# Kernel optimization log

Hardware: AMD Instinct MI355X
Metric: run time of the kernel (lower is better)

The kernel has to match this reference:

```python
import jax, jax.numpy as jnp
import numpy as np

NEG_SLOPE = 0.2

def gat_conv(x, src, dst, n_nodes, W, a_src, a_dst, bias, heads, out_c):
    # x: [N, in]; W: [in, heads*out_c]; a_src/a_dst: [heads, out_c]; bias: [heads*out_c]
    h = (x @ W).reshape(n_nodes, heads, out_c)            # [N,H,C]
    e_s = jnp.sum(h * a_src, axis=-1)                     # [N,H] per-node src score
    e_d = jnp.sum(h * a_dst, axis=-1)                     # [N,H] per-node dst score
    e = jax.nn.leaky_relu(e_s[src] + e_d[dst], NEG_SLOPE) # [E,H]
    # segment softmax over destination neighborhoods
    emax = jax.ops.segment_max(e, dst, num_segments=n_nodes)  # [N,H]
    emax = jnp.where(jnp.isfinite(emax), emax, 0.0)
    p = jnp.exp(e - emax[dst])                            # [E,H]
    denom = jax.ops.segment_sum(p, dst, num_segments=n_nodes)  # [N,H]
    alpha = p / (denom[dst] + 1e-16)                      # [E,H]
    msg = h[src] * alpha[:, :, None]                      # [E,H,C]
    out = jax.ops.segment_sum(msg, dst, num_segments=n_nodes)  # [N,H,C]
    return out.reshape(n_nodes, heads * out_c) + bias


def setup_inputs() -> dict:
    key = jax.random.key(0)
    ks = jax.random.split(key, 10)
    N, E, IN, OUT, H = 50000, 1600000, 128, 32, 2
    x = jax.random.normal(ks[0], (N, IN), dtype=jnp.float32)
    edge_index = jax.random.randint(ks[1], (2, E), 0, N, dtype=jnp.int64)
    s = 0.1
    W1 = jax.random.normal(ks[2], (IN, H * OUT), dtype=jnp.float32) * s
    a_src1 = jax.random.normal(ks[3], (H, OUT), dtype=jnp.float32) * s
    a_dst1 = jax.random.normal(ks[4], (H, OUT), dtype=jnp.float32) * s
    b1 = jnp.zeros((H * OUT,), dtype=jnp.float32)
    W2 = jax.random.normal(ks[5], (H * OUT, OUT), dtype=jnp.float32) * s
    a_src2 = jax.random.normal(ks[6], (1, OUT), dtype=jnp.float32) * s
    a_dst2 = jax.random.normal(ks[7], (1, OUT), dtype=jnp.float32) * s
    b2 = jnp.zeros((OUT,), dtype=jnp.float32)
    return {"x": x, "edge_index": edge_index, "W1": W1, "a_src1": a_src1,
            "a_dst1": a_dst1, "b1": b1, "W2": W2, "a_src2": a_src2,
            "a_dst2": a_dst2, "b2": b2}


def reference(x, edge_index, W1, a_src1, a_dst1, b1, W2, a_src2, a_dst2, b2):
    N = x.shape[0]
    # add_self_loops=True (PyG GATConv default)
    loops = jnp.arange(N, dtype=edge_index.dtype)
    ei = jnp.concatenate([edge_index, jnp.stack([loops, loops])], axis=1)
    src, dst = ei[0], ei[1]
    h = gat_conv(x, src, dst, N, W1, a_src1, a_dst1, b1, heads=2, out_c=32)
    h = jax.nn.relu(h)
    out = gat_conv(h, src, dst, N, W2, a_src2, a_dst2, b2, heads=1, out_c=32)
    return out
```

## Files before the change

kernel.cpp:

```cpp
#include <hip/hip_runtime.h>
#include <hip/hip_fp16.h>

#define NEG_SLOPE 0.2f
#define DB 128
#define NB_MAX 512
#define EPB 4096
#define CAP 8192

__global__ __launch_bounds__(256) void k_g1p(
    const float* __restrict__ x, const float* __restrict__ W,
    const float* __restrict__ a_src, const float* __restrict__ a_dst,
    __half* __restrict__ h1, float* __restrict__ es, float* __restrict__ ed, int N,
    const int* __restrict__ srcv, const int* __restrict__ dstv,
    int* __restrict__ gcur, int* __restrict__ ebuf, int E, int G1) {
  __shared__ __align__(16) char smem[32768];
  const int t = threadIdx.x;

  if ((int)blockIdx.x < G1) {
    __half* sXT = (__half*)smem;
    __half* sW  = (__half*)(smem + 16384);
    const int r0 = blockIdx.x * 64;
    {
      const float4* Wp = (const float4*)W;
#pragma unroll
      for (int i = 0; i < 8; ++i) {
        float4 v = Wp[t + i * 256];
        int fi = (t + i * 256) * 4;
        union { __half2 h2[2]; float2 f; } u;
        u.h2[0] = __float22half2_rn(make_float2(v.x, v.y));
        u.h2[1] = __float22half2_rn(make_float2(v.z, v.w));
        *(float2*)(sW + fi) = u.f;
      }
    }
    {
      int r = t & 63;
      int kq = t >> 6;
      int gr = r0 + r;
      bool ok = gr < N;
      const float* xr = x + (size_t)gr * 128;
#pragma unroll
      for (int p = 0; p < 8; ++p) {
        int k = (kq + p * 4) * 4;
        float4 v = ok ? *(const float4*)(xr + k) : make_float4(0.f, 0.f, 0.f, 0.f);
        sXT[(k + 0) * 64 + r] = __float2half(v.x);
        sXT[(k + 1) * 64 + r] = __float2half(v.y);
        sXT[(k + 2) * 64 + r] = __float2half(v.z);
        sXT[(k + 3) * 64 + r] = __float2half(v.w);
      }
    }
    __syncthreads();

    const int tx = t & 15, ty = t >> 4;
    float4 acc0 = make_float4(0.f, 0.f, 0.f, 0.f);
    float4 acc1 = acc0, acc2 = acc0, acc3 = acc0;
#pragma unroll 4
    for (int k = 0; k < 128; ++k) {
      const __half2* ap = (const __half2*)(sXT + k * 64 + ty * 4);
      const __half2* bp = (const __half2*)(sW + k * 64 + tx * 4);
      float2 a01 = __half22float2(ap[0]);
      float2 a23 = __half22float2(ap[1]);
      float2 b01 = __half22float2(bp[0]);
      float2 b23 = __half22float2(bp[1]);
      acc0.x += a01.x * b01.x; acc0.y += a01.x * b01.y; acc0.z += a01.x * b23.x; acc0.w += a01.x * b23.y;
      acc1.x += a01.y * b01.x; acc1.y += a01.y * b01.y; acc1.z += a01.y * b23.x; acc1.w += a01.y * b23.y;
      acc2.x += a23.x * b01.x; acc2.y += a23.x * b01.y; acc2.z += a23.x * b23.x; acc2.w += a23.x * b23.y;
      acc3.x += a23.y * b01.x; acc3.y += a23.y * b01.y; acc3.z += a23.y * b23.x; acc3.w += a23.y * b23.y;
    }

    float4 accs[4] = {acc0, acc1, acc2, acc3};
#pragma unroll
    for (int i = 0; i < 4; ++i) {
      int gr = r0 + ty * 4 + i;
      if (gr < N) {
        union { __half2 h[2]; float2 f; } u;
        u.h[0] = __float22half2_rn(make_float2(accs[i].x, accs[i].y));
        u.h[1] = __float22half2_rn(make_float2(accs[i].z, accs[i].w));
        *(float2*)(h1 + (size_t)gr * 64 + tx * 4) = u.f;
      }
    }

    float4 asv = *(const float4*)(a_src + tx * 4);
    float4 adv = *(const float4*)(a_dst + tx * 4);
    float esp[4], edp[4];
#pragma unroll
    for (int i = 0; i < 4; ++i) {
      esp[i] = accs[i].x * asv.x + accs[i].y * asv.y + accs[i].z * asv.z + accs[i].w * asv.w;
      edp[i] = accs[i].x * adv.x + accs[i].y * adv.y + accs[i].z * adv.z + accs[i].w * adv.w;
    }
#pragma unroll
    for (int off = 1; off <= 4; off <<= 1) {
#pragma unroll
      for (int i = 0; i < 4; ++i) {
        esp[i] += __shfl_xor(esp[i], off);
        edp[i] += __shfl_xor(edp[i], off);
      }
    }
    if ((tx & 7) == 0) {
      int hh = tx >> 3;
#pragma unroll
      for (int i = 0; i < 4; ++i) {
        int gr = r0 + ty * 4 + i;
        if (gr < N) {
          es[gr * 2 + hh] = esp[i];
          ed[gr * 2 + hh] = edp[i];
        }
      }
    }
  } else {
    int* sh    = (int*)smem;
    int* lbase = (int*)(smem + 2048);
    sh[t] = 0; sh[t + 256] = 0;
    __syncthreads();
    int base = (blockIdx.x - G1) * EPB;
    int dd[16];
#pragma unroll
    for (int i = 0; i < 16; ++i) {
      int e = base + i * 256 + t;
      dd[i] = (e < E) ? dstv[e] : -1;
      if (dd[i] >= 0) atomicAdd(&sh[dd[i] >> 7], 1);
    }
    __syncthreads();
#pragma unroll
    for (int i = 0; i < 2; ++i) {
      int b = t + 256 * i;
      int c = sh[b];
      lbase[b] = c ? (b * CAP + atomicAdd(&gcur[b], c)) : 0;
      sh[b] = 0;
    }
    __syncthreads();
#pragma unroll
    for (int i = 0; i < 16; ++i) {
      if (dd[i] >= 0) {
        int e = base + i * 256 + t;
        int b = dd[i] >> 7;
        int r = atomicAdd(&sh[b], 1);
        ebuf[lbase[b] + r] = srcv[e] | ((dd[i] & 127) << 16);
      }
    }
  }
}

__global__ __launch_bounds__(256) void k_csr(const int* __restrict__ gcur,
                                             const int* __restrict__ ebuf,
                                             int* __restrict__ rowbeg,
                                             int* __restrict__ rowend,
                                             unsigned short* __restrict__ col, int N) {
  int b = blockIdx.x;
  int cnt = gcur[b];
  int base = b * CAP;
  int dbase = b * DB;
  __shared__ int dh[DB];
  __shared__ int sc[DB];
  int t = threadIdx.x;
  if (t < DB) dh[t] = 0;
  __syncthreads();
  for (int j = t; j < cnt; j += 256) {
    int p = ebuf[base + j];
    atomicAdd(&dh[p >> 16], 1);
  }
  __syncthreads();
  int v = 0;
  if (t < DB) { v = dh[t]; sc[t] = v; }
  __syncthreads();
  for (int off = 1; off < DB; off <<= 1) {
    int u = 0;
    if (t < DB && t >= off) u = sc[t - off];
    __syncthreads();
    if (t < DB) sc[t] += u;
    __syncthreads();
  }
  if (t < DB) {
    int excl = sc[t] - v;
    int d = dbase + t;
    if (d < N) {
      rowbeg[d] = base + excl;
      rowend[d] = base + excl + v;
    }
    dh[t] = base + excl;
  }
  __syncthreads();
  for (int j = t; j < cnt; j += 256) {
    int p = ebuf[base + j];
    int r = atomicAdd(&dh[p >> 16], 1);
    col[r] = (unsigned short)(p & 0xFFFF);
  }
}

__global__ __launch_bounds__(256) void k_agg1(const int* __restrict__ rowbeg,
                                              const int* __restrict__ rowend,
                                              const unsigned short* __restrict__ col,
                                              const __half* __restrict__ h1,
                                              const float* __restrict__ es,
                                              const float* __restrict__ ed,
                                              const float* __restrict__ bias,
                                              float* __restrict__ out1, int N) {
  int d = (blockIdx.x * blockDim.x + threadIdx.x) >> 6;
  int lane = threadIdx.x & 63;
  if (d >= N) return;
  int g = lane >> 3;
  int q = lane & 7;
  int ch = q * 8;
  int hh = q >> 2;
  float edv = ed[d * 2 + hh];

  float a0 = 0.f, a1 = 0.f, a2 = 0.f, a3 = 0.f, a4 = 0.f, a5 = 0.f, a6 = 0.f, a7 = 0.f;
  float wsum = 0.f;

  if (g == 0) {
    float v = es[d * 2 + hh] + edv;
    v = v > 0.f ? v : NEG_SLOPE * v;
    float w = __expf(v);
    float4 raw = *(const float4*)(h1 + (size_t)d * 64 + ch);
    const __half2* p2 = (const __half2*)&raw;
    float2 f0 = __half22float2(p2[0]), f1 = __half22float2(p2[1]);
    float2 f2 = __half22float2(p2[2]), f3 = __half22float2(p2[3]);
    a0 = w * f0.x; a1 = w * f0.y; a2 = w * f1.x; a3 = w * f1.y;
    a4 = w * f2.x; a5 = w * f2.y; a6 = w * f3.x; a7 = w * f3.y;
    wsum = w;
  }

  int beg = rowbeg[d], end = rowend[d];
  for (int j = beg + g; j < end; j += 8) {
    int s = col[j];
    float vv = es[s * 2 + hh] + edv;
    vv = vv > 0.f ? vv : NEG_SLOPE * vv;
    float w = __expf(vv);
    float4 raw = *(const float4*)(h1 + (size_t)s * 64 + ch);
    const __half2* p2 = (const __half2*)&raw;
    float2 f0 = __half22float2(p2[0]), f1 = __half22float2(p2[1]);
    float2 f2 = __half22float2(p2[2]), f3 = __half22float2(p2[3]);
    a0 += w * f0.x; a1 += w * f0.y; a2 += w * f1.x; a3 += w * f1.y;
    a4 += w * f2.x; a5 += w * f2.y; a6 += w * f3.x; a7 += w * f3.y;
    wsum += w;
  }

#pragma unroll
  for (int off = 8; off <= 32; off <<= 1) {
    a0 += __shfl_xor(a0, off); a1 += __shfl_xor(a1, off);
    a2 += __shfl_xor(a2, off); a3 += __shfl_xor(a3, off);
    a4 += __shfl_xor(a4, off); a5 += __shfl_xor(a5, off);
    a6 += __shfl_xor(a6, off); a7 += __shfl_xor(a7, off);
    wsum += __shfl_xor(wsum, off);
  }

  if (g == 0) {
    float inv = 1.f / (wsum + 1e-16f);
    const float4 bv0 = *(const float4*)(bias + ch);
    const float4 bv1 = *(const float4*)(bias + ch + 4);
    float4 o0, o1;
    o0.x = a0 * inv + bv0.x; o0.y = a1 * inv + bv0.y;
    o0.z = a2 * inv + bv0.z; o0.w = a3 * inv + bv0.w;
    o1.x = a4 * inv + bv1.x; o1.y = a5 * inv + bv1.y;
    o1.z = a6 * inv + bv1.z; o1.w = a7 * inv + bv1.w;
    *(float4*)(out1 + (size_t)d * 64 + ch) = o0;
    *(float4*)(out1 + (size_t)d * 64 + ch + 4) = o1;
  }
}

__global__ __launch_bounds__(256) void k_gemm2(const float* __restrict__ out1,
                                               const float* __restrict__ W,
                                               const float* __restrict__ a_src,
                                               const float* __restrict__ a_dst,
                                               __half* __restrict__ hL2,
                                               float* __restrict__ es,
                                               float* __restrict__ ed, int N) {
  __shared__ float sXT[64 * 128];
  __shared__ float sW[64 * 32];
  const int t = threadIdx.x;
  const int r0 = blockIdx.x * 128;

  {
    const float4* Wp = (const float4*)W;
    float4* sWp = (float4*)sW;
#pragma unroll
    for (int i = 0; i < 2; ++i) sWp[t + i * 256] = Wp[t + i * 256];
  }
  {
    int r = t & 127;
    int kq = t >> 7;
    int gr = r0 + r;
    bool ok = gr < N;
    const float* xr = out1 + (size_t)gr * 64;
#pragma unroll
    for (int p = 0; p < 8; ++p) {
      int k = (kq + p * 2) * 4;
      float4 v = ok ? *(const float4*)(xr + k) : make_float4(0.f, 0.f, 0.f, 0.f);
      sXT[(k + 0) * 128 + r] = fmaxf(v.x, 0.f);
      sXT[(k + 1) * 128 + r] = fmaxf(v.y, 0.f);
      sXT[(k + 2) * 128 + r] = fmaxf(v.z, 0.f);
      sXT[(k + 3) * 128 + r] = fmaxf(v.w, 0.f);
    }
  }
  __syncthreads();

  const int tx = t & 7, ty = t >> 3;
  float4 acc0 = make_float4(0.f, 0.f, 0.f, 0.f);
  float4 acc1 = acc0, acc2 = acc0, acc3 = acc0;
#pragma unroll 8
  for (int k = 0; k < 64; ++k) {
    float4 av = *(const float4*)(sXT + k * 128 + ty * 4);
    float4 bv = *(const float4*)(sW + k * 32 + tx * 4);
    acc0.x += av.x * bv.x; acc0.y += av.x * bv.y; acc0.z += av.x * bv.z; acc0.w += av.x * bv.w;
    acc1.x += av.y * bv.x; acc1.y += av.y * bv.y; acc1.z += av.y * bv.z; acc1.w += av.y * bv.w;
    acc2.x += av.z * bv.x; acc2.y += av.z * bv.y; acc2.z += av.z * bv.z; acc2.w += av.z * bv.w;
    acc3.x += av.w * bv.x; acc3.y += av.w * bv.y; acc3.z += av.w * bv.z; acc3.w += av.w * bv.w;
  }

  float4 accs[4] = {acc0, acc1, acc2, acc3};
#pragma unroll
  for (int i = 0; i < 4; ++i) {
    int gr = r0 + ty * 4 + i;
    if (gr < N) {
      union { __half2 h[2]; float2 f; } u;
      u.h[0] = __float22half2_rn(make_float2(accs[i].x, accs[i].y));
      u.h[1] = __float22half2_rn(make_float2(accs[i].z, accs[i].w));
      *(float2*)(hL2 + (size_t)gr * 32 + tx * 4) = u.f;
    }
  }

  float4 asv = *(const float4*)(a_src + tx * 4);
  float4 adv = *(const float4*)(a_dst + tx * 4);
  float esp[4], edp[4];
#pragma unroll
  for (int i = 0; i < 4; ++i) {
    esp[i] = accs[i].x * asv.x + accs[i].y * asv.y + accs[i].z * asv.z + accs[i].w * asv.w;
    edp[i] = accs[i].x * adv.x + accs[i].y * adv.y + accs[i].z * adv.z + accs[i].w * adv.w;
  }
#pragma unroll
  for (int off = 1; off <= 4; off <<= 1) {
#pragma unroll
    for (int i = 0; i < 4; ++i) {
      esp[i] += __shfl_xor(esp[i], off);
      edp[i] += __shfl_xor(edp[i], off);
    }
  }
  if (tx == 0) {
#pragma unroll
    for (int i = 0; i < 4; ++i) {
      int gr = r0 + ty * 4 + i;
      if (gr < N) {
        es[gr] = esp[i];
        ed[gr] = edp[i];
      }
    }
  }
}

__global__ __launch_bounds__(256) void k_agg2(const int* __restrict__ rowbeg,
                                              const int* __restrict__ rowend,
                                              const unsigned short* __restrict__ col,
                                              const __half* __restrict__ hL2,
                                              const float* __restrict__ es,
                                              const float* __restrict__ ed,
                                              const float* __restrict__ bias,
                                              float* __restrict__ out, int N) {
  int d = (blockIdx.x * blockDim.x + threadIdx.x) >> 6;
  int lane = threadIdx.x & 63;
  if (d >= N) return;
  int g = lane >> 2;
  int q = lane & 3;
  int ch = q * 8;
  float edv = ed[d];

  float a0 = 0.f, a1 = 0.f, a2 = 0.f, a3 = 0.f, a4 = 0.f, a5 = 0.f, a6 = 0.f, a7 = 0.f;
  float wsum = 0.f;

  if (g == 0) {
    float v = es[d] + edv;
    v = v > 0.f ? v : NEG_SLOPE * v;
    float w = __expf(v);
    float4 raw = *(const float4*)(hL2 + (size_t)d * 32 + ch);
    const __half2* p2 = (const __half2*)&raw;
    float2 f0 = __half22float2(p2[0]), f1 = __half22float2(p2[1]);
    float2 f2 = __half22float2(p2[2]), f3 = __half22float2(p2[3]);
    a0 = w * f0.x; a1 = w * f0.y; a2 = w * f1.x; a3 = w * f1.y;
    a4 = w * f2.x; a5 = w * f2.y; a6 = w * f3.x; a7 = w * f3.y;
    wsum = w;
  }

  int beg = rowbeg[d], end = rowend[d];
  for (int j = beg + g; j < end; j += 16) {
    int s = col[j];
    float vv = es[s] + edv;
    vv = vv > 0.f ? vv : NEG_SLOPE * vv;
    float w = __expf(vv);
    float4 raw = *(const float4*)(hL2 + (size_t)s * 32 + ch);
    const __half2* p2 = (const __half2*)&raw;
    float2 f0 = __half22float2(p2[0]), f1 = __half22float2(p2[1]);
    float2 f2 = __half22float2(p2[2]), f3 = __half22float2(p2[3]);
    a0 += w * f0.x; a1 += w * f0.y; a2 += w * f1.x; a3 += w * f1.y;
    a4 += w * f2.x; a5 += w * f2.y; a6 += w * f3.x; a7 += w * f3.y;
    wsum += w;
  }

#pragma unroll
  for (int off = 4; off <= 32; off <<= 1) {
    a0 += __shfl_xor(a0, off); a1 += __shfl_xor(a1, off);
    a2 += __shfl_xor(a2, off); a3 += __shfl_xor(a3, off);
    a4 += __shfl_xor(a4, off); a5 += __shfl_xor(a5, off);
    a6 += __shfl_xor(a6, off); a7 += __shfl_xor(a7, off);
    wsum += __shfl_xor(wsum, off);
  }

  if (g == 0) {
    float inv = 1.f / (wsum + 1e-16f);
    const float4 bv0 = *(const float4*)(bias + ch);
    const float4 bv1 = *(const float4*)(bias + ch + 4);
    float4 o0, o1;
    o0.x = a0 * inv + bv0.x; o0.y = a1 * inv + bv0.y;
    o0.z = a2 * inv + bv0.z; o0.w = a3 * inv + bv0.w;
    o1.x = a4 * inv + bv1.x; o1.y = a5 * inv + bv1.y;
    o1.z = a6 * inv + bv1.z; o1.w = a7 * inv + bv1.w;
    *(float4*)(out + (size_t)d * 32 + ch) = o0;
    *(float4*)(out + (size_t)d * 32 + ch + 4) = o1;
  }
}

extern "C" void kernel_launch(void* const* d_in, const int* in_sizes, int n_in,
                              void* d_out, int out_size, void* d_ws, size_t ws_size,
                              hipStream_t stream) {
  const float* x      = (const float*)d_in[0];
  const int*   ei     = (const int*)d_in[1];
  const float* W1     = (const float*)d_in[2];
  const float* a_src1 = (const float*)d_in[3];
  const float* a_dst1 = (const float*)d_in[4];
  const float* b1     = (const float*)d_in[5];
  const float* W2     = (const float*)d_in[6];
  const float* a_src2 = (const float*)d_in[7];
  const float* a_dst2 = (const float*)d_in[8];
  const float* b2     = (const float*)d_in[9];
  float* out = (float*)d_out;

  const int N = in_sizes[0] / 128;
  const int E = in_sizes[1] / 2;
  const int NB = (N + DB - 1) / DB;
  const int* srcv = ei;
  const int* dstv = ei + E;

  char* base = (char*)d_ws;
  size_t off = 0;
  auto carve = [&](size_t bytes) {
    void* p = base + off;
    off += (bytes + 15) & ~(size_t)15;
    return p;
  };
  __half* h1     = (__half*)carve((size_t)N * 64 * 2);
  float*  es1    = (float*)carve((size_t)N * 2 * 4);
  float*  ed1    = (float*)carve((size_t)N * 2 * 4);
  float*  out1   = (float*)carve((size_t)N * 64 * 4);
  __half* hL2    = (__half*)carve((size_t)N * 32 * 2);
  float*  es2    = (float*)carve((size_t)N * 4);
  float*  ed2    = (float*)carve((size_t)N * 4);
  int*    gcur   = (int*)carve((size_t)NB_MAX * 4);
  int*    rowbeg = (int*)carve((size_t)N * 4);
  int*    rowend = (int*)carve((size_t)N * 4);
  unsigned short* col = (unsigned short*)carve((size_t)NB * CAP * 2);
  int*    ebuf   = (int*)carve((size_t)NB * CAP * 4);

  const int pblocks = (E + EPB - 1) / EPB;
  const int G1 = (N + 63) / 64;

  hipMemsetAsync(gcur, 0, (size_t)NB_MAX * sizeof(int), stream);

  k_g1p<<<G1 + pblocks, 256, 0, stream>>>(x, W1, a_src1, a_dst1, h1, es1, ed1, N,
                                          srcv, dstv, gcur, ebuf, E, G1);
  k_csr<<<NB, 256, 0, stream>>>(gcur, ebuf, rowbeg, rowend, col, N);

  k_agg1<<<((size_t)N * 64 + 255) / 256, 256, 0, stream>>>(rowbeg, rowend, col, h1, es1, ed1, b1, out1, N);

  k_gemm2<<<(N + 127) / 128, 256, 0, stream>>>(out1, W2, a_src2, a_dst2, hL2, es2, ed2, N);
  k_agg2<<<((size_t)N * 64 + 255) / 256, 256, 0, stream>>>(rowbeg, rowend, col, hL2, es2, ed2, b2, out, N);
}
```

Baseline: 210.1 us.

## Interleave GEMM and edge-partition blocks, halve edges per block, unroll gather loops

The fused first kernel now alternates GEMM and edge-partition work across even and odd block indices, so both kinds run together on the CUs rather than GEMM blocks first and partition blocks after. Each partition block now handles 2048 edges instead of 4096, which doubles the partition block count and the global atomics on bucket counters. The neighbor-gather loops in both aggregation kernels get an unroll-by-2 hint to keep more loads in flight. The interleaving launches some idle blocks that return at once, and the smaller partition chunks add contention on the shared bucket counters.

```diff
diff --git a/kernel.cpp b/kernel.cpp
--- a/kernel.cpp
+++ b/kernel.cpp
@@ -4,7 +4,7 @@
 #define NEG_SLOPE 0.2f
 #define DB 128
 #define NB_MAX 512
-#define EPB 4096
+#define EPB 2048
 #define CAP 8192
 
 __global__ __launch_bounds__(256) void k_g1p(
@@ -12,14 +12,18 @@
     const float* __restrict__ a_src, const float* __restrict__ a_dst,
     __half* __restrict__ h1, float* __restrict__ es, float* __restrict__ ed, int N,
     const int* __restrict__ srcv, const int* __restrict__ dstv,
-    int* __restrict__ gcur, int* __restrict__ ebuf, int E, int G1) {
+    int* __restrict__ gcur, int* __restrict__ ebuf, int E,
+    int gemmBlocks, int partBlocks) {
   __shared__ __align__(16) char smem[32768];
   const int t = threadIdx.x;
-
-  if ((int)blockIdx.x < G1) {
+  const int b = blockIdx.x;
+  const int id = b >> 1;
+
+  if ((b & 1) == 0) {
+    if (id >= gemmBlocks) return;
     __half* sXT = (__half*)smem;
     __half* sW  = (__half*)(smem + 16384);
-    const int r0 = blockIdx.x * 64;
+    const int r0 = id * 64;
     {
       const float4* Wp = (const float4*)W;
 #pragma unroll
@@ -107,14 +111,15 @@
       }
     }
   } else {
+    if (id >= partBlocks) return;
     int* sh    = (int*)smem;
     int* lbase = (int*)(smem + 2048);
     sh[t] = 0; sh[t + 256] = 0;
     __syncthreads();
-    int base = (blockIdx.x - G1) * EPB;
-    int dd[16];
-#pragma unroll
-    for (int i = 0; i < 16; ++i) {
+    int base = id * EPB;
+    int dd[8];
+#pragma unroll
+    for (int i = 0; i < 8; ++i) {
       int e = base + i * 256 + t;
       dd[i] = (e < E) ? dstv[e] : -1;
       if (dd[i] >= 0) atomicAdd(&sh[dd[i] >> 7], 1);
@@ -122,19 +127,19 @@
     __syncthreads();
 #pragma unroll
     for (int i = 0; i < 2; ++i) {
-      int b = t + 256 * i;
-      int c = sh[b];
-      lbase[b] = c ? (b * CAP + atomicAdd(&gcur[b], c)) : 0;
-      sh[b] = 0;
-    }
-    __syncthreads();
-#pragma unroll
-    for (int i = 0; i < 16; ++i) {
+      int bb = t + 256 * i;
+      int c = sh[bb];
+      lbase[bb] = c ? (bb * CAP + atomicAdd(&gcur[bb], c)) : 0;
+      sh[bb] = 0;
+    }
+    __syncthreads();
+#pragma unroll
+    for (int i = 0; i < 8; ++i) {
       if (dd[i] >= 0) {
         int e = base + i * 256 + t;
-        int b = dd[i] >> 7;
-        int r = atomicAdd(&sh[b], 1);
-        ebuf[lbase[b] + r] = srcv[e] | ((dd[i] & 127) << 16);
+        int bb = dd[i] >> 7;
+        int r = atomicAdd(&sh[bb], 1);
+        ebuf[lbase[bb] + r] = srcv[e] | ((dd[i] & 127) << 16);
       }
     }
   }
@@ -220,6 +225,7 @@
   }
 
   int beg = rowbeg[d], end = rowend[d];
+#pragma unroll 2
   for (int j = beg + g; j < end; j += 8) {
     int s = col[j];
     float vv = es[s * 2 + hh] + edv;
@@ -379,6 +385,7 @@
   }
 
   int beg = rowbeg[d], end = rowend[d];
+#pragma unroll 2
   for (int j = beg + g; j < end; j += 16) {
     int s = col[j];
     float vv = es[s] + edv;
@@ -458,12 +465,13 @@
   int*    ebuf   = (int*)carve((size_t)NB * CAP * 4);
 
   const int pblocks = (E + EPB - 1) / EPB;
-  const int G1 = (N + 63) / 64;
+  const int gemmBlocks = (N + 63) / 64;
+  const int mixBlocks = 2 * (pblocks > gemmBlocks ? pblocks : gemmBlocks);
 
   hipMemsetAsync(gcur, 0, (size_t)NB_MAX * sizeof(int), stream);
 
-  k_g1p<<<G1 + pblocks, 256, 0, stream>>>(x, W1, a_src1, a_dst1, h1, es1, ed1, N,
-                                          srcv, dstv, gcur, ebuf, E, G1);
+  k_g1p<<<mixBlocks, 256, 0, stream>>>(x, W1, a_src1, a_dst1, h1, es1, ed1, N,
+                                       srcv, dstv, gcur, ebuf, E, gemmBlocks, pblocks);
   k_csr<<<NB, 256, 0, stream>>>(gcur, ebuf, rowbeg, rowend, col, N);
 
   k_agg1<<<((size_t)N * 64 + 255) / 256, 256, 0, stream>>>(rowbeg, rowend, col, h1, es1, ed1, b1, out1, N);
```

New measurement: 210.9 us. About the same (+0.3%).
